# Kernel tuning notes

Measured on AMD Instinct MI355X. Metric: run time of the kernel, lower is better.

The kernel has to match this reference:

```python
import jax, jax.numpy as jnp
import numpy as np

ALPHA = 0.2     # LeakyReLU negative slope
NEG = -1e9      # mask value for non-edges (matches -1000000000)
N, S, O, H, E = 8192, 128, 64, 4, 262144


def setup_inputs() -> dict:
    key = jax.random.key(0)
    ks = jax.random.split(key, 6)
    x = jax.random.normal(ks[0], (1, N, S), jnp.float32)
    edges = jax.random.randint(ks[1], (2, E), 0, N, dtype=jnp.int64)
    values = jnp.ones((E,), jnp.float32)
    # xavier_normal with gain=1.414
    W_heads = jax.random.normal(ks[2], (H, S, O), jnp.float32) * (1.414 * np.sqrt(2.0 / (S + O)))
    a_heads = jax.random.normal(ks[3], (H, 2 * O), jnp.float32) * (1.414 * np.sqrt(2.0 / (1 + 2 * O)))
    lin_w = jax.random.normal(ks[4], (1, H), jnp.float32) * 0.5
    lin_b = jnp.zeros((1,), jnp.float32)
    return {"x": x, "edges": edges, "values": values, "W_heads": W_heads,
            "a_heads": a_heads, "lin_w": lin_w, "lin_b": lin_b}


def reference(x, edges, values, W_heads, a_heads, lin_w, lin_b):
    b, n, s = x.shape
    Ntot = b * n
    xf = x.reshape(Ntot, s)
    # per-head projection: [H, N, O]
    h = jnp.einsum('ns,hso->hno', xf, W_heads)
    e0, e1 = edges[0], edges[1]
    Od = h.shape[-1]
    # per-edge attention logits for all heads: a . [h_src || h_dst], shape [H, E]
    atts = (jnp.einsum('heo,ho->he', h[:, e0, :], a_heads[:, :Od])
            + jnp.einsum('heo,ho->he', h[:, e1, :], a_heads[:, Od:]))
    atts = jax.nn.leaky_relu(atts, negative_slope=ALPHA)
    # combine heads with a 1-output linear: [E]
    mt = (atts.T @ lin_w.T + lin_b)[:, 0]
    new_values = values * mt
    # scatter to dense NxN (duplicate edges sum, like sparse coo to_dense)
    dense = jnp.zeros((Ntot, Ntot), x.dtype).at[e0, e1].add(new_values)
    a_dense = jnp.zeros((Ntot, Ntot), values.dtype).at[e0, e1].add(values)
    mask = jnp.where(a_dense == 0, NEG, jnp.where(a_dense == 1, 0.0, a_dense))
    # softmax over dim 0, as in the original
    return jax.nn.softmax(dense + mask, axis=0)
```

## Files before the change

kernel.cpp:

```cpp
#include <hip/hip_runtime.h>
#include <math.h>


#define ALPHA 0.2f
constexpr int S = 128;
constexpr int O = 64;
constexpr int H = 4;
constexpr int CAP = 128;
constexpr int MAXN = 8192;

__global__ void __launch_bounds__(256) k1_scores(
    const float* __restrict__ x, const float* __restrict__ W, const float* __restrict__ a,
    float* __restrict__ s_src, float* __restrict__ s_dst,
    int* __restrict__ col_cursor, int* __restrict__ row_cursor, int* __restrict__ empty_cnt,
    int N)
{
    __shared__ float wsbuf[2 * H * S];
    int tid = threadIdx.x;
    for (int t = tid; t < 2 * H * S; t += 256) {
        int which = t / (H * S);
        int hs = t % (H * S);
        int h = hs / S, s = hs % S;
        const float* Wr = W + ((size_t)h * S + s) * O;
        const float* av = a + h * 2 * O + which * O;
        float acc = 0.f;
        for (int o = 0; o < O; ++o) acc += Wr[o] * av[o];
        wsbuf[t] = acc;
    }
    __syncthreads();
    int n = blockIdx.x * 256 + tid;
    if (n == 0) empty_cnt[0] = 0;
    if (n >= N) return;
    col_cursor[n] = 0;
    row_cursor[n] = 0;
    const float* wsrc = wsbuf;
    const float* wdst = wsbuf + H * S;
    const float4* xr = (const float4*)(x + (size_t)n * S);
    float accs[H] = {0, 0, 0, 0}, accd[H] = {0, 0, 0, 0};
    for (int i = 0; i < S / 4; ++i) {
        float4 v = xr[i];
#pragma unroll
        for (int h = 0; h < H; ++h) {
            const float* p = wsrc + h * S + i * 4;
            const float* q = wdst + h * S + i * 4;
            accs[h] += v.x * p[0] + v.y * p[1] + v.z * p[2] + v.w * p[3];
            accd[h] += v.x * q[0] + v.y * q[1] + v.z * q[2] + v.w * q[3];
        }
    }
#pragma unroll
    for (int h = 0; h < H; ++h) {
        s_src[(size_t)h * N + n] = accs[h];
        s_dst[(size_t)h * N + n] = accd[h];
    }
}

__global__ void __launch_bounds__(256) k2_scatter(
    const int* __restrict__ edges, const float* __restrict__ values,
    const float* __restrict__ s_src, const float* __restrict__ s_dst,
    const float* __restrict__ lin_w, const float* __restrict__ lin_b,
    int* __restrict__ col_cursor, int* __restrict__ row_cursor,
    int4* __restrict__ col_ent, int* __restrict__ col_r, int N, int E)
{
    int e = blockIdx.x * 256 + threadIdx.x;
    if (e >= E) return;
    int r = edges[e];
    int c = edges[(size_t)E + e];
    if ((unsigned)r >= (unsigned)N || (unsigned)c >= (unsigned)N) return;
    float mt = lin_b[0];
#pragma unroll
    for (int h = 0; h < H; ++h) {
        float att = s_src[(size_t)h * N + r] + s_dst[(size_t)h * N + c];
        att = att >= 0.f ? att : ALPHA * att;
        mt += att * lin_w[h];
    }
    float av = values[e];
    float nv = av * mt;
    int posc = atomicAdd(&col_cursor[c], 1);
    int posr = atomicAdd(&row_cursor[r], 1);
    if (posc < CAP && posr < CAP) {
        int4 ent;
        ent.x = r;
        ent.y = __float_as_int(nv);
        ent.z = __float_as_int(av);
        ent.w = r * CAP + posr;
        col_ent[(size_t)c * CAP + posc] = ent;
        col_r[(size_t)r * CAP + posr] = c;
    }
}

__global__ void __launch_bounds__(256) k3_softmax(
    const int4* __restrict__ col_ent, const int* __restrict__ col_cursor,
    float* __restrict__ val_r, int* __restrict__ empty_list, int* __restrict__ empty_cnt,
    int N)
{
    int wave = threadIdx.x >> 6, lane = threadIdx.x & 63;
    int j = blockIdx.x * 4 + wave;
    if (j >= N) return;
    int m = col_cursor[j];
    if (m > CAP) m = CAP;
    if (m == 0) {
        if (lane == 0) { int p = atomicAdd(empty_cnt, 1); empty_list[p] = j; }
        return;
    }
    const int4* base = col_ent + (size_t)j * CAP;
    if (m <= 64) {
        bool mine = lane < m;
        int r; float v, av, wlink = 0.f; int link = 0;
        if (mine) {
            int4 ent = base[lane];
            r = ent.x; v = __int_as_float(ent.y); av = __int_as_float(ent.z); link = ent.w;
        } else {
            r = -1 - lane; v = 0.f; av = 0.f;
        }
        (void)wlink;
        float dsum = 0.f, asum = 0.f;
        bool first = true;
        for (int l = 0; l < 64; ++l) {
            int rl = __shfl(r, l);
            float vl = __shfl(v, l);
            float al = __shfl(av, l);
            if (rl == r) {
                dsum += vl; asum += al;
                if (l < lane) first = false;
            }
        }
        float mask = (asum == 1.0f) ? 0.f : asum;
        float val = dsum + mask;
        float lmax = (mine && first) ? val : -INFINITY;
#pragma unroll
        for (int off = 32; off; off >>= 1) lmax = fmaxf(lmax, __shfl_xor(lmax, off));
        float ex = (mine && first) ? expf(val - lmax) : 0.f;
        float lsum = ex;
#pragma unroll
        for (int off = 32; off; off >>= 1) lsum += __shfl_xor(lsum, off);
        float inv = 1.0f / lsum;
        if (mine) val_r[link] = expf(val - lmax) * inv;
    } else {
        float lmax = -INFINITY;
        for (int k = lane; k < m; k += 64) {
            int rk = base[k].x;
            bool first = true;
            float ds = 0.f, as = 0.f;
            for (int l = 0; l < m; ++l) {
                int4 el = base[l];
                if (el.x == rk) {
                    if (l < k) first = false;
                    ds += __int_as_float(el.y);
                    as += __int_as_float(el.z);
                }
            }
            if (first) {
                float mk = (as == 1.0f) ? 0.f : as;
                lmax = fmaxf(lmax, ds + mk);
            }
        }
#pragma unroll
        for (int off = 32; off; off >>= 1) lmax = fmaxf(lmax, __shfl_xor(lmax, off));
        float lsum = 0.f;
        for (int k = lane; k < m; k += 64) {
            int rk = base[k].x;
            bool first = true;
            float ds = 0.f, as = 0.f;
            for (int l = 0; l < m; ++l) {
                int4 el = base[l];
                if (el.x == rk) {
                    if (l < k) first = false;
                    ds += __int_as_float(el.y);
                    as += __int_as_float(el.z);
                }
            }
            if (first) {
                float mk = (as == 1.0f) ? 0.f : as;
                lsum += expf(ds + mk - lmax);
            }
        }
#pragma unroll
        for (int off = 32; off; off >>= 1) lsum += __shfl_xor(lsum, off);
        float inv = 1.0f / lsum;
        for (int k = lane; k < m; k += 64) {
            int rk = base[k].x;
            float ds = 0.f, as = 0.f;
            for (int l = 0; l < m; ++l) {
                int4 el = base[l];
                if (el.x == rk) {
                    ds += __int_as_float(el.y);
                    as += __int_as_float(el.z);
                }
            }
            float mk = (as == 1.0f) ? 0.f : as;
            val_r[base[k].w] = expf(ds + mk - lmax) * inv;
        }
    }
}

__global__ void __launch_bounds__(256) k4_rowwrite(
    const int* __restrict__ col_r, const float* __restrict__ val_r,
    const int* __restrict__ row_cursor, const int* __restrict__ empty_list,
    const int* __restrict__ empty_cnt, float* __restrict__ out, int N)
{
    __shared__ float lrow[MAXN];
    int i = blockIdx.x, t = threadIdx.x;
    int n4 = N / 4;
    float4* l4 = (float4*)lrow;
    for (int k = t; k < n4; k += 256) l4[k] = make_float4(0.f, 0.f, 0.f, 0.f);
    __syncthreads();
    int mr = row_cursor[i];
    if (mr > CAP) mr = CAP;
    for (int k = t; k < mr; k += 256)
        lrow[col_r[(size_t)i * CAP + k]] = val_r[(size_t)i * CAP + k];
    int ec = empty_cnt[0];
    if (ec > 0) {
        float u = 1.0f / (float)N;
        for (int k = t; k < ec; k += 256) lrow[empty_list[k]] = u;
    }
    __syncthreads();
    float4* o4 = (float4*)(out + (size_t)i * N);
    for (int k = t; k < n4; k += 256) o4[k] = l4[k];
}

extern "C" void kernel_launch(void* const* d_in, const int* in_sizes, int n_in,
                              void* d_out, int out_size, void* d_ws, size_t ws_size,
                              hipStream_t stream) {
    const float* x = (const float*)d_in[0];
    const int* edges = (const int*)d_in[1];
    const float* values = (const float*)d_in[2];
    const float* W = (const float*)d_in[3];
    const float* a = (const float*)d_in[4];
    const float* lin_w = (const float*)d_in[5];
    const float* lin_b = (const float*)d_in[6];
    float* out = (float*)d_out;

    int N = in_sizes[0] / S;
    int E = in_sizes[2];

    char* wsb = (char*)d_ws;
    size_t off = 0;
    auto alloc = [&](size_t bytes) -> void* {
        void* p = wsb + off;
        off += (bytes + 255) & ~(size_t)255;
        return p;
    };
    float* s_src = (float*)alloc((size_t)H * N * 4);
    float* s_dst = (float*)alloc((size_t)H * N * 4);
    int* col_cursor = (int*)alloc((size_t)N * 4);
    int* row_cursor = (int*)alloc((size_t)N * 4);
    int* empty_cnt = (int*)alloc(256);
    int* empty_list = (int*)alloc((size_t)N * 4);
    int4* col_ent = (int4*)alloc((size_t)N * CAP * 16);
    int* col_r = (int*)alloc((size_t)N * CAP * 4);
    float* val_r = (float*)alloc((size_t)N * CAP * 4);

    k1_scores<<<(N + 255) / 256, 256, 0, stream>>>(x, W, a, s_src, s_dst,
                                                   col_cursor, row_cursor, empty_cnt, N);
    k2_scatter<<<(E + 255) / 256, 256, 0, stream>>>(edges, values, s_src, s_dst, lin_w, lin_b,
                                                    col_cursor, row_cursor, col_ent, col_r, N, E);
    k3_softmax<<<(N + 3) / 4, 256, 0, stream>>>(col_ent, col_cursor, val_r,
                                                empty_list, empty_cnt, N);
    k4_rowwrite<<<N, 256, 0, stream>>>(col_r, val_r, row_cursor, empty_list, empty_cnt, out, N);
}
```

Before: 120.6 us.

## Write dense output rows directly to global and pack per-node head scores as float4

The row-write kernel no longer stages each 8192-wide row in 32KB of shared memory. It zero-fills the output row in global memory, synchronises, then scatters the row's edge values and the empty-column fill straight into global memory, handling four rows per block. Separately, the per-node source and destination head scores are stored as one float4 per node, so the edge kernel gathers them with two vector loads instead of eight scalar loads. The goal is to remove the shared-memory occupancy limit and the extra LDS copy pass on the output write, which dominates the runtime. The cost is that scattered global writes can land on cache lines that were just zero-filled, and correctness relies on the block barrier ordering those global writes.

```diff
diff --git a/kernel.cpp b/kernel.cpp
--- a/kernel.cpp
+++ b/kernel.cpp
@@ -7,11 +7,11 @@
 constexpr int O = 64;
 constexpr int H = 4;
 constexpr int CAP = 128;
-constexpr int MAXN = 8192;
+constexpr int RPB = 4;
 
 __global__ void __launch_bounds__(256) k1_scores(
     const float* __restrict__ x, const float* __restrict__ W, const float* __restrict__ a,
-    float* __restrict__ s_src, float* __restrict__ s_dst,
+    float4* __restrict__ s_src4, float4* __restrict__ s_dst4,
     int* __restrict__ col_cursor, int* __restrict__ row_cursor, int* __restrict__ empty_cnt,
     int N)
 {
@@ -47,16 +47,13 @@
             accd[h] += v.x * q[0] + v.y * q[1] + v.z * q[2] + v.w * q[3];
         }
     }
-#pragma unroll
-    for (int h = 0; h < H; ++h) {
-        s_src[(size_t)h * N + n] = accs[h];
-        s_dst[(size_t)h * N + n] = accd[h];
-    }
+    s_src4[n] = make_float4(accs[0], accs[1], accs[2], accs[3]);
+    s_dst4[n] = make_float4(accd[0], accd[1], accd[2], accd[3]);
 }
 
 __global__ void __launch_bounds__(256) k2_scatter(
     const int* __restrict__ edges, const float* __restrict__ values,
-    const float* __restrict__ s_src, const float* __restrict__ s_dst,
+    const float4* __restrict__ s_src4, const float4* __restrict__ s_dst4,
     const float* __restrict__ lin_w, const float* __restrict__ lin_b,
     int* __restrict__ col_cursor, int* __restrict__ row_cursor,
     int4* __restrict__ col_ent, int* __restrict__ col_r, int N, int E)
@@ -66,13 +63,14 @@
     int r = edges[e];
     int c = edges[(size_t)E + e];
     if ((unsigned)r >= (unsigned)N || (unsigned)c >= (unsigned)N) return;
-    float mt = lin_b[0];
-#pragma unroll
-    for (int h = 0; h < H; ++h) {
-        float att = s_src[(size_t)h * N + r] + s_dst[(size_t)h * N + c];
-        att = att >= 0.f ? att : ALPHA * att;
-        mt += att * lin_w[h];
-    }
+    float4 ss = s_src4[r];
+    float4 sd = s_dst4[c];
+    float att0 = ss.x + sd.x, att1 = ss.y + sd.y, att2 = ss.z + sd.z, att3 = ss.w + sd.w;
+    att0 = att0 >= 0.f ? att0 : ALPHA * att0;
+    att1 = att1 >= 0.f ? att1 : ALPHA * att1;
+    att2 = att2 >= 0.f ? att2 : ALPHA * att2;
+    att3 = att3 >= 0.f ? att3 : ALPHA * att3;
+    float mt = lin_b[0] + att0 * lin_w[0] + att1 * lin_w[1] + att2 * lin_w[2] + att3 * lin_w[3];
     float av = values[e];
     float nv = av * mt;
     int posc = atomicAdd(&col_cursor[c], 1);
@@ -105,14 +103,13 @@
     const int4* base = col_ent + (size_t)j * CAP;
     if (m <= 64) {
         bool mine = lane < m;
-        int r; float v, av, wlink = 0.f; int link = 0;
+        int r; float v, av; int link = 0;
         if (mine) {
             int4 ent = base[lane];
             r = ent.x; v = __int_as_float(ent.y); av = __int_as_float(ent.z); link = ent.w;
         } else {
             r = -1 - lane; v = 0.f; av = 0.f;
         }
-        (void)wlink;
         float dsum = 0.f, asum = 0.f;
         bool first = true;
         for (int l = 0; l < 64; ++l) {
@@ -198,24 +195,26 @@
     const int* __restrict__ row_cursor, const int* __restrict__ empty_list,
     const int* __restrict__ empty_cnt, float* __restrict__ out, int N)
 {
-    __shared__ float lrow[MAXN];
-    int i = blockIdx.x, t = threadIdx.x;
+    int t = threadIdx.x;
+    const float4 z4 = make_float4(0.f, 0.f, 0.f, 0.f);
+    int ec = empty_cnt[0];
+    float u = 1.0f / (float)N;
     int n4 = N / 4;
-    float4* l4 = (float4*)lrow;
-    for (int k = t; k < n4; k += 256) l4[k] = make_float4(0.f, 0.f, 0.f, 0.f);
-    __syncthreads();
-    int mr = row_cursor[i];
-    if (mr > CAP) mr = CAP;
-    for (int k = t; k < mr; k += 256)
-        lrow[col_r[(size_t)i * CAP + k]] = val_r[(size_t)i * CAP + k];
-    int ec = empty_cnt[0];
-    if (ec > 0) {
-        float u = 1.0f / (float)N;
-        for (int k = t; k < ec; k += 256) lrow[empty_list[k]] = u;
-    }
-    __syncthreads();
-    float4* o4 = (float4*)(out + (size_t)i * N);
-    for (int k = t; k < n4; k += 256) o4[k] = l4[k];
+#pragma unroll
+    for (int q = 0; q < RPB; ++q) {
+        int i = blockIdx.x * RPB + q;
+        if (i >= N) return;
+        float* orow = out + (size_t)i * N;
+        float4* o4 = (float4*)orow;
+        for (int k = t; k < n4; k += 256) o4[k] = z4;
+        __syncthreads();
+        int mr = row_cursor[i];
+        if (mr > CAP) mr = CAP;
+        const int* cr = col_r + (size_t)i * CAP;
+        const float* vr = val_r + (size_t)i * CAP;
+        for (int k = t; k < mr; k += 256) orow[cr[k]] = vr[k];
+        for (int k = t; k < ec; k += 256) orow[empty_list[k]] = u;
+    }
 }
 
 extern "C" void kernel_launch(void* const* d_in, const int* in_sizes, int n_in,
@@ -240,8 +239,8 @@
         off += (bytes + 255) & ~(size_t)255;
         return p;
     };
-    float* s_src = (float*)alloc((size_t)H * N * 4);
-    float* s_dst = (float*)alloc((size_t)H * N * 4);
+    float4* s_src4 = (float4*)alloc((size_t)N * 16);
+    float4* s_dst4 = (float4*)alloc((size_t)N * 16);
     int* col_cursor = (int*)alloc((size_t)N * 4);
     int* row_cursor = (int*)alloc((size_t)N * 4);
     int* empty_cnt = (int*)alloc(256);
@@ -250,11 +249,12 @@
     int* col_r = (int*)alloc((size_t)N * CAP * 4);
     float* val_r = (float*)alloc((size_t)N * CAP * 4);
 
-    k1_scores<<<(N + 255) / 256, 256, 0, stream>>>(x, W, a, s_src, s_dst,
+    k1_scores<<<(N + 255) / 256, 256, 0, stream>>>(x, W, a, s_src4, s_dst4,
                                                    col_cursor, row_cursor, empty_cnt, N);
-    k2_scatter<<<(E + 255) / 256, 256, 0, stream>>>(edges, values, s_src, s_dst, lin_w, lin_b,
+    k2_scatter<<<(E + 255) / 256, 256, 0, stream>>>(edges, values, s_src4, s_dst4, lin_w, lin_b,
                                                     col_cursor, row_cursor, col_ent, col_r, N, E);
     k3_softmax<<<(N + 3) / 4, 256, 0, stream>>>(col_ent, col_cursor, val_r,
                                                 empty_list, empty_cnt, N);
-    k4_rowwrite<<<N, 256, 0, stream>>>(col_r, val_r, row_cursor, empty_list, empty_cnt, out, N);
-}
+    k4_rowwrite<<<(N + RPB - 1) / RPB, 256, 0, stream>>>(col_r, val_r, row_cursor,
+                                                         empty_list, empty_cnt, out, N);
+}
```

After: 121.0 us. Within noise of the previous version (+0.3%).
